# Kernel optimization log

Measured on AMD Instinct MI355X. Metric: run time of the kernel, lower is better.

The kernel has to match this reference:

```python
import jax, jax.numpy as jnp
import numpy as np

NUM_EXPERTS = 8
TOP_K = 2
ENTROPY_WEIGHT = 0.1
MAX_USAGE_RATIO = 0.3


def setup_inputs() -> dict:
    key = jax.random.key(0)
    k0, k1, k2 = jax.random.split(key, 3)
    B, S, D, H, E = 4, 4096, 1024, 1024, NUM_EXPERTS
    x = jax.random.normal(k0, (B, S, D), jnp.float32)
    gate_w = jax.random.normal(k1, (D, E), jnp.float32) * (1.0 / np.sqrt(D))
    gate_b = jnp.zeros((E,), jnp.float32)
    expert_w = jax.random.normal(k2, (E, D, H), jnp.float32) * (1.0 / np.sqrt(D))
    expert_b = jnp.zeros((E, H), jnp.float32)
    return {"x": x, "gate_w": gate_w, "gate_b": gate_b,
            "expert_w": expert_w, "expert_b": expert_b}


def reference(x, gate_w, gate_b, expert_w, expert_b):
    # x: [B, S, D]; dropout omitted (eval mode / deterministic reference)
    B, S, D = x.shape
    E = gate_w.shape[1]
    H = expert_w.shape[2]
    N = B * S
    xf = x.reshape(N, D)

    gate_logits = xf @ gate_w + gate_b            # [N, E]
    gate_probs = jax.nn.softmax(gate_logits, axis=-1)
    entropy = -jnp.sum(gate_probs * jnp.log(gate_probs + 1e-10), axis=-1).mean()
    entropy_loss = ENTROPY_WEIGHT * entropy

    topk_probs, topk_idx = jax.lax.top_k(gate_probs, TOP_K)   # [N, K]
    onehot = jax.nn.one_hot(topk_idx, E, dtype=xf.dtype)       # [N, K, E]
    combine = jnp.einsum('nk,nke->ne', topk_probs, onehot)     # [N, E] gating weight per expert

    # Weighted combine of per-expert Linear outputs; loop over small fixed E.
    out = jnp.zeros((N, H), xf.dtype)
    for e in range(E):
        out = out + combine[:, e:e + 1] * (xf @ expert_w[e] + expert_b[e])

    counts = jnp.sum(onehot, axis=(0, 1))                      # [E] tokens routed per expert
    usage_ratios = counts / N
    overuse_penalty = jnp.sum(jax.nn.relu(usage_ratios - MAX_USAGE_RATIO))

    return out.reshape(B, S, H), entropy_loss + overuse_penalty
```

## Files before the change

### kernel.cpp

```cpp
#include <hip/hip_runtime.h>
#include <hip/hip_bf16.h>

typedef __bf16 bf16x8 __attribute__((ext_vector_type(8)));
typedef __bf16 bf16x4 __attribute__((ext_vector_type(4)));
typedef float  f32x4  __attribute__((ext_vector_type(4)));

#define NTOK 16384
#define DDIM 1024
#define HDIM 1024
#define CNT_STRIDE 16

#define XB_OFF   0u
#define WT_OFF   33554432u
#define IDXP_OFF 50331648u
#define PPP_OFF  50397184u
#define TPID_OFF 50528256u
#define TPP_OFF  50593792u
#define CNT_OFF  50724864u
#define CUR_OFF  50728960u
#define BASE_OFF 50733056u
#define TILT_OFF 50733312u
#define NT_OFF   50736384u
#define ENT_OFF  50736388u
#define ZERO_LEN 11536u

typedef __attribute__((address_space(1))) void gvoid_t;
typedef __attribute__((address_space(3))) void lvoid_t;

__device__ __forceinline__ void cp16(void* lds, const void* g) {
  __builtin_amdgcn_global_load_lds((gvoid_t*)g, (lvoid_t*)lds, 16, 0, 0);
}

__global__ __launch_bounds__(256) void transpose_w(const float* __restrict__ w,
                                                   __bf16* __restrict__ wT) {
  const int b  = blockIdx.x;
  const int e  = b >> 8;
  const int d0 = ((b >> 4) & 15) * 64;
  const int h0 = (b & 15) * 64;
  __shared__ float tile[64][69];
  const int t = threadIdx.x;
  const float* base = w + ((size_t)e * DDIM + d0) * HDIM + h0;
#pragma unroll
  for (int it = 0; it < 4; ++it) {
    int dl = it * 16 + (t >> 4);
    int hl = (t & 15) * 4;
    float4 v = *(const float4*)(base + (size_t)dl * HDIM + hl);
    tile[dl][hl]     = v.x;
    tile[dl][hl + 1] = v.y;
    tile[dl][hl + 2] = v.z;
    tile[dl][hl + 3] = v.w;
  }
  __syncthreads();
  __bf16* obase = wT + ((size_t)e * HDIM + h0) * DDIM + d0;
#pragma unroll
  for (int it = 0; it < 2; ++it) {
    int hl = it * 32 + (t >> 3);
    int dl = (t & 7) * 8;
    bf16x8 bv;
#pragma unroll
    for (int i = 0; i < 8; ++i) bv[i] = (__bf16)tile[dl + i][hl];
    *(bf16x8*)(obase + (size_t)hl * DDIM + dl) = bv;
  }
}

__global__ __launch_bounds__(256) void gate_kernel(
    const float* __restrict__ x, const float* __restrict__ gw,
    const float* __restrict__ gb, __bf16* __restrict__ xb,
    int* __restrict__ tt_pid, float2* __restrict__ tt_pp,
    int* __restrict__ cnt_g, float* __restrict__ ent_g) {
  __shared__ float gwT[8 * 1024];
  __shared__ int   lcnt[64];
  __shared__ float went[4];
  const int tid = threadIdx.x, w = tid >> 6, lane = tid & 63;
  for (int i = tid; i < 64; i += 256) lcnt[i] = 0;
#pragma unroll
  for (int i = 0; i < 32; ++i) {
    int lin = i * 256 + tid;
    gwT[(lin & 7) * 1024 + (lin >> 3)] = gw[lin];
  }
  __syncthreads();
  float4 gr[4][8];
#pragma unroll
  for (int j = 0; j < 4; ++j)
#pragma unroll
    for (int e = 0; e < 8; ++e)
      gr[j][e] = *(const float4*)&gwT[e * 1024 + j * 256 + lane * 4];
  float gbr[8];
#pragma unroll
  for (int e = 0; e < 8; ++e) gbr[e] = gb[e];

  float entacc = 0.f;
  for (int t = 0; t < 4; ++t) {
    const int n = blockIdx.x * 16 + w * 4 + t;
    float acc[8] = {0.f, 0.f, 0.f, 0.f, 0.f, 0.f, 0.f, 0.f};
#pragma unroll
    for (int j = 0; j < 4; ++j) {
      float4 v = *(const float4*)(x + (size_t)n * DDIM + j * 256 + lane * 4);
      bf16x4 bv;
      bv[0] = (__bf16)v.x; bv[1] = (__bf16)v.y;
      bv[2] = (__bf16)v.z; bv[3] = (__bf16)v.w;
      *(bf16x4*)(xb + (size_t)n * DDIM + j * 256 + lane * 4) = bv;
#pragma unroll
      for (int e = 0; e < 8; ++e) {
        float4 g = gr[j][e];
        acc[e] += v.x * g.x + v.y * g.y + v.z * g.z + v.w * g.w;
      }
    }
#pragma unroll
    for (int e = 0; e < 8; ++e) {
      float s = acc[e];
#pragma unroll
      for (int off = 1; off < 64; off <<= 1) s += __shfl_xor(s, off);
      acc[e] = s;
    }
    float p[8], lg[8];
    float mx = -1e30f;
#pragma unroll
    for (int e = 0; e < 8; ++e) { p[e] = acc[e] + gbr[e]; mx = fmaxf(mx, p[e]); }
    float s = 0.f;
#pragma unroll
    for (int e = 0; e < 8; ++e) { lg[e] = p[e] - mx; p[e] = expf(lg[e]); s += p[e]; }
    float inv = 1.0f / s;
    float dot = 0.f;
#pragma unroll
    for (int e = 0; e < 8; ++e) { p[e] *= inv; dot += p[e] * lg[e]; }
    entacc += logf(s) - dot;
    int e1 = 0; float p1 = p[0];
#pragma unroll
    for (int e = 1; e < 8; ++e) if (p[e] > p1) { p1 = p[e]; e1 = e; }
    int e2 = (e1 == 0) ? 1 : 0; float p2 = p[e2];
#pragma unroll
    for (int e = 0; e < 8; ++e) if (e != e1 && p[e] > p2) { p2 = p[e]; e2 = e; }
    int   elo = (e1 < e2) ? e1 : e2;
    int   ehi = (e1 < e2) ? e2 : e1;
    float plo = (e1 < e2) ? p1 : p2;
    float phi = (e1 < e2) ? p2 : p1;
    int pid = elo * 8 + ehi;
    if (lane == 0) {
      tt_pid[n] = pid;
      tt_pp[n]  = make_float2(plo, phi);
      atomicAdd(&lcnt[pid], 1);
    }
  }
  if (lane == 0) went[w] = entacc;
  __syncthreads();
  if (tid < 64 && lcnt[tid]) atomicAdd(&cnt_g[tid * CNT_STRIDE], lcnt[tid]);
  if (tid == 0)
    atomicAdd(ent_g, went[0] + went[1] + went[2] + went[3]);
}

__global__ void scan_kernel(const int* __restrict__ cnt_g, int* __restrict__ base_g,
                            int4* __restrict__ tilt, int* __restrict__ nt_g,
                            const float* __restrict__ ent_g, float* __restrict__ loss_out) {
  __shared__ int csh[64];
  const int t = threadIdx.x;
  csh[t] = cnt_g[t * CNT_STRIDE];
  __syncthreads();
  if (t == 0) {
    int b = 0, ti = 0;
    int ecnt[8] = {0, 0, 0, 0, 0, 0, 0, 0};
    for (int pid = 0; pid < 64; ++pid) {
      int c = csh[pid];
      base_g[pid] = b;
      if (c > 0) {
        ecnt[pid >> 3] += c;
        ecnt[pid & 7]  += c;
        for (int r = 0; r < c; r += 128) tilt[ti++] = make_int4(pid, r, c, b);
        b += c;
      }
    }
    *nt_g = ti;
    float pen = 0.f;
    for (int e = 0; e < 8; ++e) {
      float r = (float)ecnt[e] / (float)NTOK - 0.3f;
      if (r > 0.f) pen += r;
    }
    loss_out[0] = 0.1f * (ent_g[0] / (float)NTOK) + pen;
  }
}

__global__ __launch_bounds__(256) void scatter_kernel(
    const int* __restrict__ tt_pid, const float2* __restrict__ tt_pp,
    const int* __restrict__ base_g, int* __restrict__ cur_g,
    int* __restrict__ idx_p, float2* __restrict__ pp_p) {
  __shared__ int lcnt[64], lbase[64];
  const int tid = threadIdx.x;
  if (tid < 64) lcnt[tid] = 0;
  __syncthreads();
  const int n = blockIdx.x * 256 + tid;
  const int pid = tt_pid[n];
  int lofs = atomicAdd(&lcnt[pid], 1);
  __syncthreads();
  if (tid < 64 && lcnt[tid]) lbase[tid] = atomicAdd(&cur_g[tid * CNT_STRIDE], lcnt[tid]);
  __syncthreads();
  int dst = base_g[pid] + lbase[pid] + lofs;
  idx_p[dst] = n;
  pp_p[dst]  = tt_pp[n];
}

__global__ __launch_bounds__(256) void moe_gemm(
    const __bf16* __restrict__ xb, const __bf16* __restrict__ wT,
    const float* __restrict__ eb, const int* __restrict__ idx_p,
    const float2* __restrict__ pp_p, const int4* __restrict__ tilt,
    const int* __restrict__ nt_g, float* __restrict__ out) {
  const int gy = blockIdx.y;
  if (gy >= *nt_g) return;
  const int4 te = tilt[gy];
  const int pid = te.x, row0 = te.y, cntp = te.z, gbase = te.w;
  const int elo = pid >> 3, ehi = pid & 7;
  const int gx = blockIdx.x;

  __shared__ __bf16 Ash [2][128 * 64];
  __shared__ __bf16 BloS[2][128 * 64];
  __shared__ __bf16 BhiS[2][128 * 64];
  __shared__ int    tok_s[128];
  __shared__ float2 pp_s[128];

  const int tid = threadIdx.x, w = tid >> 6, lane = tid & 63;
  if (tid < 128) {
    int s = row0 + tid;
    int g = gbase + ((s < cntp) ? s : (cntp - 1));
    tok_s[tid] = idx_p[g];
    pp_s[tid]  = pp_p[g];
  }
  __syncthreads();

  f32x4 accL[4][4], accH[4][4];
  const f32x4 zero = {0.f, 0.f, 0.f, 0.f};
#pragma unroll
  for (int mi = 0; mi < 4; ++mi)
#pragma unroll
    for (int ni = 0; ni < 4; ++ni) { accL[mi][ni] = zero; accH[mi][ni] = zero; }

  const int wm = (w >> 1) * 64, wn = (w & 1) * 64;
  const int tq = lane >> 4, tr = lane & 15, tr7 = tr & 7;
  const int rsub = lane >> 3;
  const int csw = ((lane & 7) ^ rsub) * 8;

  const __bf16* wlo = wT + (size_t)elo * HDIM * DDIM + (size_t)(gx * 128) * DDIM;
  const __bf16* whi = wT + (size_t)ehi * HDIM * DDIM + (size_t)(gx * 128) * DDIM;
  const __bf16* aptr[4];
  const __bf16* lptr[4];
  const __bf16* hptr[4];
#pragma unroll
  for (int it = 0; it < 4; ++it) {
    int r = it * 32 + w * 8 + rsub;
    aptr[it] = xb + (size_t)tok_s[r] * DDIM + csw;
    lptr[it] = wlo + (size_t)r * DDIM + csw;
    hptr[it] = whi + (size_t)r * DDIM + csw;
  }

#pragma unroll
  for (int it = 0; it < 4; ++it) {
    const int rb = it * 32 + w * 8;
    cp16((char*)Ash[0]  + rb * 128, aptr[it]); aptr[it] += 64;
    cp16((char*)BloS[0] + rb * 128, lptr[it]); lptr[it] += 64;
    cp16((char*)BhiS[0] + rb * 128, hptr[it]); hptr[it] += 64;
  }
  __syncthreads();

  int cur = 0;
  for (int kk = 0; kk < 16; ++kk) {
    if (kk < 15) {
#pragma unroll
      for (int it = 0; it < 4; ++it) {
        const int rb = it * 32 + w * 8;
        cp16((char*)Ash[cur ^ 1]  + rb * 128, aptr[it]); aptr[it] += 64;
        cp16((char*)BloS[cur ^ 1] + rb * 128, lptr[it]); lptr[it] += 64;
        cp16((char*)BhiS[cur ^ 1] + rb * 128, hptr[it]); hptr[it] += 64;
      }
    }

#pragma unroll
    for (int h = 0; h < 2; ++h) {
      const int co = (h << 2) | tq;
      bf16x8 a[4], bl[4], bh[4];
#pragma unroll
      for (int mi = 0; mi < 4; ++mi)
        a[mi] = *(const bf16x8*)((const char*)Ash[cur] + (wm + mi * 16 + tr) * 128 +
                                 ((co ^ tr7) << 4));
#pragma unroll
      for (int ni = 0; ni < 4; ++ni) {
        bl[ni] = *(const bf16x8*)((const char*)BloS[cur] + (wn + ni * 16 + tr) * 128 +
                                  ((co ^ tr7) << 4));
        bh[ni] = *(const bf16x8*)((const char*)BhiS[cur] + (wn + ni * 16 + tr) * 128 +
                                  ((co ^ tr7) << 4));
      }
#pragma unroll
      for (int mi = 0; mi < 4; ++mi)
#pragma unroll
        for (int ni = 0; ni < 4; ++ni) {
          accL[mi][ni] = __builtin_amdgcn_mfma_f32_16x16x32_bf16(a[mi], bl[ni], accL[mi][ni], 0, 0, 0);
          accH[mi][ni] = __builtin_amdgcn_mfma_f32_16x16x32_bf16(a[mi], bh[ni], accH[mi][ni], 0, 0, 0);
        }
    }

    if (kk < 15) { __syncthreads(); cur ^= 1; }
  }

  float blov[4], bhiv[4];
#pragma unroll
  for (int ni = 0; ni < 4; ++ni) {
    int col = gx * 128 + wn + ni * 16 + tr;
    blov[ni] = eb[elo * HDIM + col];
    bhiv[ni] = eb[ehi * HDIM + col];
  }
#pragma unroll
  for (int mi = 0; mi < 4; ++mi)
#pragma unroll
    for (int r = 0; r < 4; ++r) {
      int lr = wm + mi * 16 + tq * 4 + r;
      if (row0 + lr < cntp) {
        int    tok = tok_s[lr];
        float2 pp  = pp_s[lr];
        float* orow = out + (size_t)tok * HDIM + gx * 128 + wn + tr;
#pragma unroll
        for (int ni = 0; ni < 4; ++ni)
          orow[ni * 16] = pp.x * (accL[mi][ni][r] + blov[ni]) +
                          pp.y * (accH[mi][ni][r] + bhiv[ni]);
      }
    }
}

extern "C" void kernel_launch(void* const* d_in, const int* in_sizes, int n_in,
                              void* d_out, int out_size, void* d_ws, size_t ws_size,
                              hipStream_t stream) {
  const float* x  = (const float*)d_in[0];
  const float* gw = (const float*)d_in[1];
  const float* gb = (const float*)d_in[2];
  const float* ew = (const float*)d_in[3];
  const float* eb = (const float*)d_in[4];
  float* out = (float*)d_out;
  char*  ws  = (char*)d_ws;

  __bf16* xb     = (__bf16*)(ws + XB_OFF);
  __bf16* wT     = (__bf16*)(ws + WT_OFF);
  int*    idx_p  = (int*)(ws + IDXP_OFF);
  float2* pp_p   = (float2*)(ws + PPP_OFF);
  int*    tt_pid = (int*)(ws + TPID_OFF);
  float2* tt_pp  = (float2*)(ws + TPP_OFF);
  int*    cnt_g  = (int*)(ws + CNT_OFF);
  int*    cur_g  = (int*)(ws + CUR_OFF);
  int*    base_g = (int*)(ws + BASE_OFF);
  int4*   tilt   = (int4*)(ws + TILT_OFF);
  int*    nt_g   = (int*)(ws + NT_OFF);
  float*  ent_g  = (float*)(ws + ENT_OFF);

  hipMemsetAsync(ws + CNT_OFF, 0, ZERO_LEN, stream);
  transpose_w<<<dim3(2048), 256, 0, stream>>>(ew, wT);
  gate_kernel<<<dim3(1024), 256, 0, stream>>>(x, gw, gb, xb, tt_pid, tt_pp,
                                              cnt_g, ent_g);
  scan_kernel<<<1, 64, 0, stream>>>(cnt_g, base_g, tilt, nt_g, ent_g,
                                    out + (size_t)NTOK * HDIM);
  scatter_kernel<<<dim3(64), 256, 0, stream>>>(tt_pid, tt_pp, base_g, cur_g,
                                               idx_p, pp_p);
  moe_gemm<<<dim3(8, 160), 256, 0, stream>>>(xb, wT, eb, idx_p, pp_p, tilt,
                                             nt_g, out);
}
```

Measured before the change: 341.8 us.

## Single-buffer MoE GEMM LDS, swizzle tile order, fold memset into transpose

Drops the double-buffered LDS staging in the MoE GEMM to a single buffer (halving LDS use, from 96KB to 48KB plus token metadata) so more workgroups can be resident per CU, at the cost of losing the copy/compute overlap within a block. Remaps the launch grid so groups of 8 consecutive row tiles share each column tile, which is meant to improve L2 reuse. Replaces the separate hipMemsetAsync with zeroing done by block 0 of the transpose kernel to save a launch.

```diff
diff --git a/kernel.cpp b/kernel.cpp
--- a/kernel.cpp
+++ b/kernel.cpp
@@ -4,6 +4,7 @@
 typedef __bf16 bf16x8 __attribute__((ext_vector_type(8)));
 typedef __bf16 bf16x4 __attribute__((ext_vector_type(4)));
 typedef float  f32x4  __attribute__((ext_vector_type(4)));
+typedef int    i32x4  __attribute__((ext_vector_type(4)));
 
 #define NTOK 16384
 #define DDIM 1024
@@ -32,13 +33,19 @@
 }
 
 __global__ __launch_bounds__(256) void transpose_w(const float* __restrict__ w,
-                                                   __bf16* __restrict__ wT) {
+                                                   __bf16* __restrict__ wT,
+                                                   int* __restrict__ zero_base) {
+  const int t = threadIdx.x;
+  if (blockIdx.x == 0) {
+    i32x4* z = (i32x4*)zero_base;
+    const i32x4 zz = {0, 0, 0, 0};
+    for (int i = t; i < (int)(ZERO_LEN / 16); i += 256) z[i] = zz;
+  }
   const int b  = blockIdx.x;
   const int e  = b >> 8;
   const int d0 = ((b >> 4) & 15) * 64;
   const int h0 = (b & 15) * 64;
   __shared__ float tile[64][69];
-  const int t = threadIdx.x;
   const float* base = w + ((size_t)e * DDIM + d0) * HDIM + h0;
 #pragma unroll
   for (int it = 0; it < 4; ++it) {
@@ -203,16 +210,17 @@
     const float* __restrict__ eb, const int* __restrict__ idx_p,
     const float2* __restrict__ pp_p, const int4* __restrict__ tilt,
     const int* __restrict__ nt_g, float* __restrict__ out) {
-  const int gy = blockIdx.y;
+  const int lin = blockIdx.y * 8 + blockIdx.x;
+  const int gy  = (lin & 7) + 8 * (lin >> 6);
+  const int gx  = (lin >> 3) & 7;
   if (gy >= *nt_g) return;
   const int4 te = tilt[gy];
   const int pid = te.x, row0 = te.y, cntp = te.z, gbase = te.w;
   const int elo = pid >> 3, ehi = pid & 7;
-  const int gx = blockIdx.x;
-
-  __shared__ __bf16 Ash [2][128 * 64];
-  __shared__ __bf16 BloS[2][128 * 64];
-  __shared__ __bf16 BhiS[2][128 * 64];
+
+  __shared__ __bf16 Ash[128 * 64];
+  __shared__ __bf16 BloS[128 * 64];
+  __shared__ __bf16 BhiS[128 * 64];
   __shared__ int    tok_s[128];
   __shared__ float2 pp_s[128];
 
@@ -250,40 +258,28 @@
     hptr[it] = whi + (size_t)r * DDIM + csw;
   }
 
-#pragma unroll
-  for (int it = 0; it < 4; ++it) {
-    const int rb = it * 32 + w * 8;
-    cp16((char*)Ash[0]  + rb * 128, aptr[it]); aptr[it] += 64;
-    cp16((char*)BloS[0] + rb * 128, lptr[it]); lptr[it] += 64;
-    cp16((char*)BhiS[0] + rb * 128, hptr[it]); hptr[it] += 64;
-  }
-  __syncthreads();
-
-  int cur = 0;
   for (int kk = 0; kk < 16; ++kk) {
-    if (kk < 15) {
-#pragma unroll
-      for (int it = 0; it < 4; ++it) {
-        const int rb = it * 32 + w * 8;
-        cp16((char*)Ash[cur ^ 1]  + rb * 128, aptr[it]); aptr[it] += 64;
-        cp16((char*)BloS[cur ^ 1] + rb * 128, lptr[it]); lptr[it] += 64;
-        cp16((char*)BhiS[cur ^ 1] + rb * 128, hptr[it]); hptr[it] += 64;
-      }
-    }
-
+#pragma unroll
+    for (int it = 0; it < 4; ++it) {
+      const int rb = it * 32 + w * 8;
+      cp16((char*)Ash  + rb * 128, aptr[it]); aptr[it] += 64;
+      cp16((char*)BloS + rb * 128, lptr[it]); lptr[it] += 64;
+      cp16((char*)BhiS + rb * 128, hptr[it]); hptr[it] += 64;
+    }
+    __syncthreads();
 #pragma unroll
     for (int h = 0; h < 2; ++h) {
       const int co = (h << 2) | tq;
       bf16x8 a[4], bl[4], bh[4];
 #pragma unroll
       for (int mi = 0; mi < 4; ++mi)
-        a[mi] = *(const bf16x8*)((const char*)Ash[cur] + (wm + mi * 16 + tr) * 128 +
+        a[mi] = *(const bf16x8*)((const char*)Ash + (wm + mi * 16 + tr) * 128 +
                                  ((co ^ tr7) << 4));
 #pragma unroll
       for (int ni = 0; ni < 4; ++ni) {
-        bl[ni] = *(const bf16x8*)((const char*)BloS[cur] + (wn + ni * 16 + tr) * 128 +
+        bl[ni] = *(const bf16x8*)((const char*)BloS + (wn + ni * 16 + tr) * 128 +
                                   ((co ^ tr7) << 4));
-        bh[ni] = *(const bf16x8*)((const char*)BhiS[cur] + (wn + ni * 16 + tr) * 128 +
+        bh[ni] = *(const bf16x8*)((const char*)BhiS + (wn + ni * 16 + tr) * 128 +
                                   ((co ^ tr7) << 4));
       }
 #pragma unroll
@@ -294,8 +290,7 @@
           accH[mi][ni] = __builtin_amdgcn_mfma_f32_16x16x32_bf16(a[mi], bh[ni], accH[mi][ni], 0, 0, 0);
         }
     }
-
-    if (kk < 15) { __syncthreads(); cur ^= 1; }
+    __syncthreads();
   }
 
   float blov[4], bhiv[4];
@@ -346,8 +341,7 @@
   int*    nt_g   = (int*)(ws + NT_OFF);
   float*  ent_g  = (float*)(ws + ENT_OFF);
 
-  hipMemsetAsync(ws + CNT_OFF, 0, ZERO_LEN, stream);
-  transpose_w<<<dim3(2048), 256, 0, stream>>>(ew, wT);
+  transpose_w<<<dim3(2048), 256, 0, stream>>>(ew, wT, cnt_g);
   gate_kernel<<<dim3(1024), 256, 0, stream>>>(x, gw, gb, xb, tt_pid, tt_pp,
                                               cnt_g, ent_g);
   scan_kernel<<<1, 64, 0, stream>>>(cnt_g, base_g, tilt, nt_g, ent_g,
```

Result: faster. 323.4 us (-5.4%).
